# Kernel optimization log

Hardware: AMD Instinct MI355X
Metric: run time of the kernel (lower is better)

## Reference

```python
import jax, jax.numpy as jnp
import numpy as np

IN_FEATURES = 256
OUT_FEATURES = 256
GRID_SIZE = 5
SPLINE_ORDER = 3  # k


def setup_inputs() -> dict:
    key = jax.random.key(0)
    k1, k2, k3, k4 = jax.random.split(key, 4)
    x = jax.random.uniform(k1, (1024, IN_FEATURES), dtype=jnp.float32)  # in [0,1) subset of grid_range
    base_weight = jax.random.normal(k2, (IN_FEATURES, OUT_FEATURES), dtype=jnp.float32) * 0.05
    n_basis = GRID_SIZE + SPLINE_ORDER - 1  # 7
    spline_weight = jax.random.normal(k3, (IN_FEATURES, OUT_FEATURES, n_basis), dtype=jnp.float32) * 0.05
    # grid: (grid_size, in_features); sorted per feature inside grid_range (-1,1)
    grid = jnp.sort(jax.random.uniform(k4, (GRID_SIZE, IN_FEATURES), dtype=jnp.float32, minval=-1.0, maxval=1.0), axis=0)
    return {"x": x, "base_weight": base_weight, "spline_weight": spline_weight, "grid": grid}


def _safe_div(num, den):
    # B-spline convention: 0/0 terms contribute 0 (repeated knots from constant-fill grid extension).
    ok = den != 0
    return jnp.where(ok, num / jnp.where(ok, den, 1.0), 0.0)


def _bspline_basis(x, grid, k):
    # x: (b, in); grid: (G, in) -> basis (b, in, G+k-1) via Cox-de Boor recursion.
    gt = grid.T  # (in, G)
    left = jnp.repeat(2.0 * gt[:, :1] - gt[:, k:k + 1], k, axis=1)       # k copies of 2*g0 - g_k
    right = jnp.repeat(2.0 * gt[:, -1:] - gt[:, -k - 1:-k], k, axis=1)   # k copies of 2*g_-1 - g_{-k-1}
    eg = jnp.concatenate([left, gt, right], axis=1)  # (in, G+2k) extended grid
    xe = x[:, :, None]  # (b, in, 1)
    B = ((xe >= eg[None, :, :-1]) & (xe < eg[None, :, 1:])).astype(x.dtype)  # order-1 indicator basis
    for d in range(1, k):
        lt = _safe_div(xe - eg[None, :, :-d - 1], (eg[:, d:-1] - eg[:, :-d - 1])[None])
        rt = _safe_div(eg[None, :, d + 1:] - xe, (eg[:, d + 1:] - eg[:, 1:-d])[None])
        B = lt * B[..., :-1] + rt * B[..., 1:]
    return B[..., :grid.shape[0] + k - 1]  # first G+k-1 functions, matching spline_weight's last dim


def reference(x, base_weight, spline_weight, grid):
    k = SPLINE_ORDER
    basis = _bspline_basis(x, grid, k)                     # (b, in, K)
    base_out = x @ base_weight                             # (b, out)
    spline_out = jnp.einsum('bik,iok->bio', basis, spline_weight)  # (b, in, out)
    # base_out (b,out) broadcasts against (b,in,out), as in the original tf code
    return jax.nn.silu(base_out[:, None, :] + spline_out)
```

## Files before the change

### kernel.cpp

```cpp
#include <hip/hip_runtime.h>
#include <math.h>


#define B_TOT 1024
#define NF 256

__device__ __forceinline__ float silu_f(float z) {
    float e = __expf(-z);
    return z * __builtin_amdgcn_rcpf(1.0f + e);
}

__global__ __launch_bounds__(256) void base_gemm(const float* __restrict__ x,
                                                 const float* __restrict__ W,
                                                 float* __restrict__ base) {
    __shared__ float xs[2][NF];
    const int b0 = blockIdx.x * 2;
    const int t = threadIdx.x;
    xs[0][t] = x[(b0 + 0) * NF + t];
    xs[1][t] = x[(b0 + 1) * NF + t];
    __syncthreads();
    float acc0 = 0.f, acc1 = 0.f;
#pragma unroll 8
    for (int k = 0; k < NF; ++k) {
        float w = W[k * NF + t];
        acc0 += xs[0][k] * w;
        acc1 += xs[1][k] * w;
    }
    base[(b0 + 0) * NF + t] = acc0;
    base[(b0 + 1) * NF + t] = acc1;
}

__global__ __launch_bounds__(256) void kan_main(const float* __restrict__ x,
                                                const float* __restrict__ sw,
                                                const float* __restrict__ grid,
                                                const float* __restrict__ base,
                                                float* __restrict__ out) {
    const int i0 = blockIdx.x * 16;
    const int b0 = blockIdx.y * 16;
    const int tid = threadIdx.x;

    __shared__ float bas[16][16][8];

    {
        const int ii = tid & 15;
        const int bb = tid >> 4;
        const int gi = i0 + ii;
        const float xv = x[(b0 + bb) * NF + gi];
        const float g0 = grid[0 * NF + gi];
        const float g1 = grid[1 * NF + gi];
        const float g2 = grid[2 * NF + gi];
        const float g3 = grid[3 * NF + gi];
        const float g4 = grid[4 * NF + gi];
        const float L = 2.f * g0 - g3;
        const float R = 2.f * g4 - g1;
        float eg[11] = {L, L, L, g0, g1, g2, g3, g4, R, R, R};

        float B0[10];
#pragma unroll
        for (int t = 0; t < 10; ++t)
            B0[t] = (xv >= eg[t] && xv < eg[t + 1]) ? 1.f : 0.f;

        float B1[9];
#pragma unroll
        for (int t = 0; t < 9; ++t) {
            float dl = eg[t + 1] - eg[t];
            float dr = eg[t + 2] - eg[t + 1];
            float lt = (dl != 0.f) ? (xv - eg[t]) / dl : 0.f;
            float rt = (dr != 0.f) ? (eg[t + 2] - xv) / dr : 0.f;
            B1[t] = lt * B0[t] + rt * B0[t + 1];
        }
        float B2[8];
#pragma unroll
        for (int t = 0; t < 8; ++t) {
            float dl = eg[t + 2] - eg[t];
            float dr = eg[t + 3] - eg[t + 1];
            float lt = (dl != 0.f) ? (xv - eg[t]) / dl : 0.f;
            float rt = (dr != 0.f) ? (eg[t + 3] - xv) / dr : 0.f;
            B2[t] = lt * B1[t] + rt * B1[t + 1];
        }
#pragma unroll
        for (int k = 0; k < 7; ++k) bas[ii][bb][k] = B2[k];
        bas[ii][bb][7] = 0.f;
    }

    const int lane = tid & 63;
    const int wv = tid >> 6;
    float4 br[16];
#pragma unroll
    for (int bb = 0; bb < 16; ++bb)
        br[bb] = *reinterpret_cast<const float4*>(&base[(size_t)(b0 + bb) * NF + lane * 4]);

    __syncthreads();

    for (int step = 0; step < 4; ++step) {
        const int ii = wv * 4 + step;
        const int i = i0 + ii;

        float s[4][7];
#pragma unroll
        for (int oo = 0; oo < 4; ++oo) {
            const float* p = &sw[((size_t)i * NF + lane * 4 + oo) * 7];
#pragma unroll
            for (int k = 0; k < 7; ++k) s[oo][k] = p[k];
        }

#pragma unroll
        for (int bb = 0; bb < 16; ++bb) {
            float4 bl = *reinterpret_cast<const float4*>(&bas[ii][bb][0]);
            float4 bh = *reinterpret_cast<const float4*>(&bas[ii][bb][4]);
            float bk[7] = {bl.x, bl.y, bl.z, bl.w, bh.x, bh.y, bh.z};
            float a0 = br[bb].x, a1 = br[bb].y, a2 = br[bb].z, a3 = br[bb].w;
#pragma unroll
            for (int k = 0; k < 7; ++k) {
                a0 += bk[k] * s[0][k];
                a1 += bk[k] * s[1][k];
                a2 += bk[k] * s[2][k];
                a3 += bk[k] * s[3][k];
            }
            float4 o4;
            o4.x = silu_f(a0);
            o4.y = silu_f(a1);
            o4.z = silu_f(a2);
            o4.w = silu_f(a3);
            *reinterpret_cast<float4*>(
                &out[((size_t)(b0 + bb) * NF + i) * NF + lane * 4]) = o4;
        }
    }
}

extern "C" void kernel_launch(void* const* d_in, const int* in_sizes, int n_in,
                              void* d_out, int out_size, void* d_ws, size_t ws_size,
                              hipStream_t stream) {
    const float* x    = (const float*)d_in[0];
    const float* bw   = (const float*)d_in[1];
    const float* sw   = (const float*)d_in[2];
    const float* grid = (const float*)d_in[3];
    float* out = (float*)d_out;
    float* base = (float*)d_ws;

    base_gemm<<<dim3(512), 256, 0, stream>>>(x, bw, base);
    kan_main<<<dim3(16, 64), 256, 0, stream>>>(x, sw, grid, base, out);
}
```

Before: 64.59 us.

## Halve batch tile, stage base in LDS, vectorize weight loads, nontemporal output stores

Shrinks the per-block batch chunk from 16 to 8 rows and doubles the grid, so there are more blocks. The base GEMM rows are staged in shared memory instead of held in registers, and spline weights are loaded as seven float4 vectors instead of scalar loads. The large output is written with nontemporal stores to avoid polluting the cache. The trade-off is that each weight load is reused over fewer batch rows, and only half the threads compute basis values.

```diff
diff --git a/kernel.cpp b/kernel.cpp
--- a/kernel.cpp
+++ b/kernel.cpp
@@ -2,8 +2,11 @@
 #include <math.h>
 
 
-#define B_TOT 1024
 #define NF 256
+#define BCH 8
+#define ICH 16
+
+typedef float f32x4 __attribute__((ext_vector_type(4)));
 
 __device__ __forceinline__ float silu_f(float z) {
     float e = __expf(-z);
@@ -35,17 +38,27 @@
                                                 const float* __restrict__ grid,
                                                 const float* __restrict__ base,
                                                 float* __restrict__ out) {
-    const int i0 = blockIdx.x * 16;
-    const int b0 = blockIdx.y * 16;
+    const int i0 = blockIdx.x * ICH;
+    const int b0 = blockIdx.y * BCH;
     const int tid = threadIdx.x;
 
-    __shared__ float bas[16][16][8];
+    __shared__ float bas[ICH][BCH][8];
+    __shared__ float base_s[BCH][NF];
 
-    {
-        const int ii = tid & 15;
+#pragma unroll
+    for (int r = 0; r < 2; ++r) {
+        const int f4 = tid + r * 256;
+        const int row = f4 >> 6;
+        const int c4 = (f4 & 63) * 4;
+        *reinterpret_cast<f32x4*>(&base_s[row][c4]) =
+            *reinterpret_cast<const f32x4*>(&base[(size_t)(b0 + row) * NF + c4]);
+    }
+
+    if (tid < ICH * BCH) {
+        const int ii = tid & (ICH - 1);
         const int bb = tid >> 4;
         const int gi = i0 + ii;
-        const float xv = x[(b0 + bb) * NF + gi];
+        const float xv = x[(size_t)(b0 + bb) * NF + gi];
         const float g0 = grid[0 * NF + gi];
         const float g1 = grid[1 * NF + gi];
         const float g2 = grid[2 * NF + gi];
@@ -59,7 +72,6 @@
 #pragma unroll
         for (int t = 0; t < 10; ++t)
             B0[t] = (xv >= eg[t] && xv < eg[t + 1]) ? 1.f : 0.f;
-
         float B1[9];
 #pragma unroll
         for (int t = 0; t < 9; ++t) {
@@ -83,47 +95,50 @@
         bas[ii][bb][7] = 0.f;
     }
 
+    __syncthreads();
+
     const int lane = tid & 63;
     const int wv = tid >> 6;
-    float4 br[16];
-#pragma unroll
-    for (int bb = 0; bb < 16; ++bb)
-        br[bb] = *reinterpret_cast<const float4*>(&base[(size_t)(b0 + bb) * NF + lane * 4]);
-
-    __syncthreads();
 
     for (int step = 0; step < 4; ++step) {
         const int ii = wv * 4 + step;
         const int i = i0 + ii;
 
-        float s[4][7];
+        f32x4 q[7];
+        const f32x4* p4 = reinterpret_cast<const f32x4*>(
+            &sw[((size_t)i * NF + lane * 4) * 7]);
 #pragma unroll
-        for (int oo = 0; oo < 4; ++oo) {
-            const float* p = &sw[((size_t)i * NF + lane * 4 + oo) * 7];
+        for (int j = 0; j < 7; ++j) q[j] = p4[j];
+        float s[28];
 #pragma unroll
-            for (int k = 0; k < 7; ++k) s[oo][k] = p[k];
+        for (int j = 0; j < 7; ++j) {
+            s[j * 4 + 0] = q[j].x; s[j * 4 + 1] = q[j].y;
+            s[j * 4 + 2] = q[j].z; s[j * 4 + 3] = q[j].w;
         }
 
+        float* op = out + ((size_t)b0 * NF + i) * NF + lane * 4;
+
 #pragma unroll
-        for (int bb = 0; bb < 16; ++bb) {
-            float4 bl = *reinterpret_cast<const float4*>(&bas[ii][bb][0]);
-            float4 bh = *reinterpret_cast<const float4*>(&bas[ii][bb][4]);
-            float bk[7] = {bl.x, bl.y, bl.z, bl.w, bh.x, bh.y, bh.z};
-            float a0 = br[bb].x, a1 = br[bb].y, a2 = br[bb].z, a3 = br[bb].w;
+        for (int bb = 0; bb < BCH; ++bb) {
+            f32x4 bl = *reinterpret_cast<const f32x4*>(&bas[ii][bb][0]);
+            f32x4 bh = *reinterpret_cast<const f32x4*>(&bas[ii][bb][4]);
+            const float bk[7] = {bl.x, bl.y, bl.z, bl.w, bh.x, bh.y, bh.z};
+            f32x4 bs = *reinterpret_cast<const f32x4*>(&base_s[bb][lane * 4]);
+            float a0 = bs.x, a1 = bs.y, a2 = bs.z, a3 = bs.w;
 #pragma unroll
             for (int k = 0; k < 7; ++k) {
-                a0 += bk[k] * s[0][k];
-                a1 += bk[k] * s[1][k];
-                a2 += bk[k] * s[2][k];
-                a3 += bk[k] * s[3][k];
+                a0 += bk[k] * s[0 * 7 + k];
+                a1 += bk[k] * s[1 * 7 + k];
+                a2 += bk[k] * s[2 * 7 + k];
+                a3 += bk[k] * s[3 * 7 + k];
             }
-            float4 o4;
+            f32x4 o4;
             o4.x = silu_f(a0);
             o4.y = silu_f(a1);
             o4.z = silu_f(a2);
             o4.w = silu_f(a3);
-            *reinterpret_cast<float4*>(
-                &out[((size_t)(b0 + bb) * NF + i) * NF + lane * 4]) = o4;
+            __builtin_nontemporal_store(o4,
+                reinterpret_cast<f32x4*>(op + (size_t)bb * NF * NF));
         }
     }
 }
@@ -139,5 +154,5 @@
     float* base = (float*)d_ws;
 
     base_gemm<<<dim3(512), 256, 0, stream>>>(x, bw, base);
-    kan_main<<<dim3(16, 64), 256, 0, stream>>>(x, sw, grid, base, out);
+    kan_main<<<dim3(16, 128), 256, 0, stream>>>(x, sw, grid, base, out);
 }
```

Result: slower. 69.00 us (+6.8%).
